# Kernel tuning notes

Hardware: AMD Instinct MI355X
Metric: run time of the kernel (lower is better)

## Reference

```python
import jax, jax.numpy as jnp
import numpy as np

N_NODES = 2048
N_ELEMS = 4096

# kind codes
KIND_R, KIND_IVS, KIND_VC, KIND_SW = 0, 1, 2, 3


def setup_inputs() -> dict:
    key = jax.random.key(0)
    k1, k2, k3 = jax.random.split(key, 3)
    M = jax.random.normal(k1, (N_NODES, N_ELEMS), dtype=jnp.float32)
    params = jax.random.uniform(k2, (N_ELEMS,), dtype=jnp.float32)
    kinds = jax.random.randint(k3, (N_ELEMS,), 0, 4, dtype=jnp.int32)
    return {"M": M, "params": params, "kinds": kinds}


def reference(M, params, kinds):
    N, E = M.shape
    W = 2 * E + N  # column width of every row block
    dt = M.dtype

    # kcl rows: [M | 0_{N,E} | 0_{N,N}]
    kcl = jnp.concatenate([M, jnp.zeros((N, E + N), dtype=dt)], axis=1)
    # kvl rows: [0_{E,E} | I_E | -M^T]
    kvl = jnp.concatenate(
        [jnp.zeros((E, E), dtype=dt), jnp.eye(E, dtype=dt), -M.T], axis=1
    )

    is_r = kinds == KIND_R
    is_ivs = kinds == KIND_IVS
    is_vc = kinds == KIND_VC
    is_sw = kinds == KIND_SW
    sw_on = params > 0

    one = jnp.ones((), dtype=dt)
    zero = jnp.zeros((), dtype=dt)
    # z-column value at pos: R -> -param, VC -> 1, SW(off) -> 1, else 0
    z_val = jnp.where(is_r, -params,
             jnp.where(is_vc | (is_sw & ~sw_on), one, zero)).astype(dt)
    # y-column value at E+pos: R -> 1, IVS -> 1, SW(on) -> 1, else 0
    y_val = jnp.where(is_r | is_ivs | (is_sw & sw_on), one, zero).astype(dt)

    pos = jnp.arange(E)
    elem = jnp.zeros((E, W), dtype=dt)
    elem = elem.at[pos, pos].set(z_val)
    elem = elem.at[pos, E + pos].set(y_val)

    return jnp.concatenate([kcl, kvl, elem], axis=0)
```

## Files before the change

kernel.cpp:

```cpp
#include <hip/hip_runtime.h>

#define NN 2048
#define EE 4096
#define WW 10240
#define TOT_ROWS 10240

typedef float v4f __attribute__((ext_vector_type(4)));

#define TP_BLOCKS 2048

__global__ __launch_bounds__(256) void coeff_kernel(
    const float* __restrict__ M,
    const float* __restrict__ params,
    const int*   __restrict__ kinds,
    float*       __restrict__ out)
{
    int tid = threadIdx.x;

    if (blockIdx.x < TP_BLOCKS) {
        __shared__ __align__(16) float t[64 * 64];
        int cTile = (blockIdx.x & 63) << 6;
        int rTile = (blockIdx.x >> 6) << 6;
        int r = tid & 15, q = tid >> 4;
        int c0 = r * 4;

        #pragma unroll
        for (int it = 0; it < 4; ++it) {
            int lrow = it * 16 + q;
            v4f val = *(const v4f*)(M + (size_t)(rTile + lrow) * EE + cTile + c0);
            *(v4f*)(out + (size_t)(rTile + lrow) * WW + cTile + c0) = val;
            #pragma unroll
            for (int s = 0; s < 4; ++s) {
                int i = (s + (r >> 2)) & 3;
                int c = c0 + i;
                t[c * 64 + (lrow ^ ((c & 15) * 4))] = val[i];
            }
        }
        __syncthreads();

        #pragma unroll
        for (int it = 0; it < 4; ++it) {
            int e  = it * 16 + q;
            int j0 = r * 4;
            v4f v = *(const v4f*)(t + e * 64 + (j0 ^ ((e & 15) * 4)));
            v4f nv = { -v[0], -v[1], -v[2], -v[3] };
            *(v4f*)(out + (size_t)(NN + cTile + e) * WW + 2 * EE + rTile + j0) = nv;
        }
    } else {
        int row = blockIdx.x - TP_BLOCKS;
        float* dst = out + (size_t)row * WW;
        const v4f zero = {0.f, 0.f, 0.f, 0.f};

        if (row < NN) {
            #pragma unroll
            for (int k = 4; k < 10; ++k)
                *(v4f*)(dst + (k * 256 + tid) * 4) = zero;
        } else if (row < NN + EE) {
            int e = row - NN;
            int col_y = EE + e;
            #pragma unroll
            for (int k = 0; k < 8; ++k) {
                int base = (k * 256 + tid) * 4;
                v4f v = zero;
                #pragma unroll
                for (int j = 0; j < 4; ++j)
                    if (base + j == col_y) v[j] = 1.0f;
                *(v4f*)(dst + base) = v;
            }
        } else {
            int e = row - (NN + EE);
            float p = params[e];
            int kk = kinds[e];
            bool on = p > 0.0f;
            float z, y;
            if (kk == 0)      { z = -p;             y = 1.0f; }
            else if (kk == 1) { z = 0.0f;           y = 1.0f; }
            else if (kk == 2) { z = 1.0f;           y = 0.0f; }
            else              { z = on ? 0.f : 1.f; y = on ? 1.f : 0.f; }
            int col_z = e, col_y = EE + e;
            #pragma unroll
            for (int k = 0; k < 10; ++k) {
                int base = (k * 256 + tid) * 4;
                v4f v = zero;
                #pragma unroll
                for (int j = 0; j < 4; ++j) {
                    if (base + j == col_z) v[j] = z;
                    if (base + j == col_y) v[j] = y;
                }
                *(v4f*)(dst + base) = v;
            }
        }
    }
}

extern "C" void kernel_launch(void* const* d_in, const int* in_sizes, int n_in,
                              void* d_out, int out_size, void* d_ws, size_t ws_size,
                              hipStream_t stream) {
    const float* M      = (const float*)d_in[0];
    const float* params = (const float*)d_in[1];
    const int*   kinds  = (const int*)d_in[2];
    float*       out    = (float*)d_out;

    coeff_kernel<<<TP_BLOCKS + TOT_ROWS, 256, 0, stream>>>(M, params, kinds, out);
}
```

Before: 434.2 us.

## Split into row-fill and transpose kernels with wider 64x256 transpose tiles

The single fused kernel becomes two launches. A row kernel writes every output row, including the copy of M into the KCL rows. A separate transpose kernel writes -M^T using 64x256 tiles held in 64KB of shared memory, so each output row segment is 1KB of contiguous stores instead of 256B. The cost is a second kernel launch with serialization between the two, lower occupancy from the larger shared memory tile, and M being read twice.

```diff
diff --git a/kernel.cpp b/kernel.cpp
--- a/kernel.cpp
+++ b/kernel.cpp
@@ -7,88 +7,101 @@
 
 typedef float v4f __attribute__((ext_vector_type(4)));
 
-#define TP_BLOCKS 2048
-
-__global__ __launch_bounds__(256) void coeff_kernel(
+__global__ __launch_bounds__(256) void row_kernel(
     const float* __restrict__ M,
     const float* __restrict__ params,
     const int*   __restrict__ kinds,
     float*       __restrict__ out)
 {
+    int row = blockIdx.x;
     int tid = threadIdx.x;
+    float* dst = out + (size_t)row * WW;
+    const v4f zero = {0.f, 0.f, 0.f, 0.f};
 
-    if (blockIdx.x < TP_BLOCKS) {
-        __shared__ __align__(16) float t[64 * 64];
-        int cTile = (blockIdx.x & 63) << 6;
-        int rTile = (blockIdx.x >> 6) << 6;
-        int r = tid & 15, q = tid >> 4;
-        int c0 = r * 4;
+    if (row < NN) {
+        const float* src = M + (size_t)row * EE;
+        #pragma unroll
+        for (int k = 0; k < 4; ++k) {
+            int off = (k * 256 + tid) * 4;
+            *(v4f*)(dst + off) = *(const v4f*)(src + off);
+        }
+        #pragma unroll
+        for (int k = 4; k < 10; ++k)
+            *(v4f*)(dst + (k * 256 + tid) * 4) = zero;
+    } else if (row < NN + EE) {
+        int e = row - NN;
+        int col_y = EE + e;
+        #pragma unroll
+        for (int k = 0; k < 8; ++k) {
+            int base = (k * 256 + tid) * 4;
+            v4f v = zero;
+            #pragma unroll
+            for (int j = 0; j < 4; ++j)
+                if (base + j == col_y) v[j] = 1.0f;
+            *(v4f*)(dst + base) = v;
+        }
+    } else {
+        int e = row - (NN + EE);
+        float p = params[e];
+        int kk = kinds[e];
+        bool on = p > 0.0f;
+        float z, y;
+        if (kk == 0)      { z = -p;             y = 1.0f; }
+        else if (kk == 1) { z = 0.0f;           y = 1.0f; }
+        else if (kk == 2) { z = 1.0f;           y = 0.0f; }
+        else              { z = on ? 0.f : 1.f; y = on ? 1.f : 0.f; }
+        int col_z = e, col_y = EE + e;
+        #pragma unroll
+        for (int k = 0; k < 10; ++k) {
+            int base = (k * 256 + tid) * 4;
+            v4f v = zero;
+            #pragma unroll
+            for (int j = 0; j < 4; ++j) {
+                if (base + j == col_z) v[j] = z;
+                if (base + j == col_y) v[j] = y;
+            }
+            *(v4f*)(dst + base) = v;
+        }
+    }
+}
 
+__global__ __launch_bounds__(256) void tp_kernel(
+    const float* __restrict__ M,
+    float*       __restrict__ out)
+{
+    __shared__ __align__(16) float t[4][64 * 64];
+    int cT = blockIdx.x << 6;
+    int rT = blockIdx.y << 8;
+    int tid = threadIdx.x;
+    int r = tid & 15, q = tid >> 4;
+    int c0 = r * 4;
+
+    #pragma unroll
+    for (int w = 0; w < 4; ++w) {
         #pragma unroll
         for (int it = 0; it < 4; ++it) {
             int lrow = it * 16 + q;
-            v4f val = *(const v4f*)(M + (size_t)(rTile + lrow) * EE + cTile + c0);
-            *(v4f*)(out + (size_t)(rTile + lrow) * WW + cTile + c0) = val;
+            v4f val = *(const v4f*)(M + (size_t)(rT + w * 64 + lrow) * EE + cT + c0);
             #pragma unroll
             for (int s = 0; s < 4; ++s) {
                 int i = (s + (r >> 2)) & 3;
                 int c = c0 + i;
-                t[c * 64 + (lrow ^ ((c & 15) * 4))] = val[i];
+                t[w][c * 64 + (lrow ^ ((c & 15) * 4))] = val[i];
             }
         }
-        __syncthreads();
+    }
+    __syncthreads();
 
+    #pragma unroll
+    for (int it = 0; it < 4; ++it) {
+        int e  = it * 16 + q;
+        int j0 = r * 4;
+        float* dst = out + (size_t)(NN + cT + e) * WW + 2 * EE + rT + j0;
         #pragma unroll
-        for (int it = 0; it < 4; ++it) {
-            int e  = it * 16 + q;
-            int j0 = r * 4;
-            v4f v = *(const v4f*)(t + e * 64 + (j0 ^ ((e & 15) * 4)));
+        for (int w = 0; w < 4; ++w) {
+            v4f v = *(const v4f*)(&t[w][e * 64 + (j0 ^ ((e & 15) * 4))]);
             v4f nv = { -v[0], -v[1], -v[2], -v[3] };
-            *(v4f*)(out + (size_t)(NN + cTile + e) * WW + 2 * EE + rTile + j0) = nv;
-        }
-    } else {
-        int row = blockIdx.x - TP_BLOCKS;
-        float* dst = out + (size_t)row * WW;
-        const v4f zero = {0.f, 0.f, 0.f, 0.f};
-
-        if (row < NN) {
-            #pragma unroll
-            for (int k = 4; k < 10; ++k)
-                *(v4f*)(dst + (k * 256 + tid) * 4) = zero;
-        } else if (row < NN + EE) {
-            int e = row - NN;
-            int col_y = EE + e;
-            #pragma unroll
-            for (int k = 0; k < 8; ++k) {
-                int base = (k * 256 + tid) * 4;
-                v4f v = zero;
-                #pragma unroll
-                for (int j = 0; j < 4; ++j)
-                    if (base + j == col_y) v[j] = 1.0f;
-                *(v4f*)(dst + base) = v;
-            }
-        } else {
-            int e = row - (NN + EE);
-            float p = params[e];
-            int kk = kinds[e];
-            bool on = p > 0.0f;
-            float z, y;
-            if (kk == 0)      { z = -p;             y = 1.0f; }
-            else if (kk == 1) { z = 0.0f;           y = 1.0f; }
-            else if (kk == 2) { z = 1.0f;           y = 0.0f; }
-            else              { z = on ? 0.f : 1.f; y = on ? 1.f : 0.f; }
-            int col_z = e, col_y = EE + e;
-            #pragma unroll
-            for (int k = 0; k < 10; ++k) {
-                int base = (k * 256 + tid) * 4;
-                v4f v = zero;
-                #pragma unroll
-                for (int j = 0; j < 4; ++j) {
-                    if (base + j == col_z) v[j] = z;
-                    if (base + j == col_y) v[j] = y;
-                }
-                *(v4f*)(dst + base) = v;
-            }
+            *(v4f*)(dst + w * 64) = nv;
         }
     }
 }
@@ -101,5 +114,6 @@
     const int*   kinds  = (const int*)d_in[2];
     float*       out    = (float*)d_out;
 
-    coeff_kernel<<<TP_BLOCKS + TOT_ROWS, 256, 0, stream>>>(M, params, kinds, out);
+    row_kernel<<<TOT_ROWS, 256, 0, stream>>>(M, params, kinds, out);
+    tp_kernel<<<dim3(EE / 64, NN / 256), 256, 0, stream>>>(M, out);
 }
```

Measured after the change: 443.5 us. 2.2% more time.

## Use nontemporal stores and enlarge transpose tiles to 64x256 per block

Applied to the files above, without the earlier changes.

All output writes now use nontemporal vector stores, to avoid polluting caches with the large write-only output. The transpose blocks each handle four 64x64 tiles along the node dimension, so each transposed row segment is 256 contiguous floats. This cuts the transpose block count by four. The larger shared buffer (64KB) reduces how many transpose blocks can be resident per CU.

```diff
diff --git a/kernel.cpp b/kernel.cpp
--- a/kernel.cpp
+++ b/kernel.cpp
@@ -7,7 +7,11 @@
 
 typedef float v4f __attribute__((ext_vector_type(4)));
 
-#define TP_BLOCKS 2048
+#define TP_BLOCKS 512
+
+__device__ __forceinline__ void nt_store(float* p, v4f v) {
+    __builtin_nontemporal_store(v, (v4f*)p);
+}
 
 __global__ __launch_bounds__(256) void coeff_kernel(
     const float* __restrict__ M,
@@ -18,22 +22,26 @@
     int tid = threadIdx.x;
 
     if (blockIdx.x < TP_BLOCKS) {
-        __shared__ __align__(16) float t[64 * 64];
-        int cTile = (blockIdx.x & 63) << 6;
-        int rTile = (blockIdx.x >> 6) << 6;
+        __shared__ __align__(16) float t[4][64 * 64];
+        int cT = (blockIdx.x & 63) << 6;
+        int rT = (blockIdx.x >> 6) << 8;
         int r = tid & 15, q = tid >> 4;
         int c0 = r * 4;
 
         #pragma unroll
-        for (int it = 0; it < 4; ++it) {
-            int lrow = it * 16 + q;
-            v4f val = *(const v4f*)(M + (size_t)(rTile + lrow) * EE + cTile + c0);
-            *(v4f*)(out + (size_t)(rTile + lrow) * WW + cTile + c0) = val;
+        for (int w = 0; w < 4; ++w) {
             #pragma unroll
-            for (int s = 0; s < 4; ++s) {
-                int i = (s + (r >> 2)) & 3;
-                int c = c0 + i;
-                t[c * 64 + (lrow ^ ((c & 15) * 4))] = val[i];
+            for (int it = 0; it < 4; ++it) {
+                int lrow = it * 16 + q;
+                int grow = rT + w * 64 + lrow;
+                v4f val = *(const v4f*)(M + (size_t)grow * EE + cT + c0);
+                nt_store(out + (size_t)grow * WW + cT + c0, val);
+                #pragma unroll
+                for (int s = 0; s < 4; ++s) {
+                    int i = (s + (r >> 2)) & 3;
+                    int c = c0 + i;
+                    t[w][c * 64 + (lrow ^ ((c & 15) * 4))] = val[i];
+                }
             }
         }
         __syncthreads();
@@ -42,30 +50,35 @@
         for (int it = 0; it < 4; ++it) {
             int e  = it * 16 + q;
             int j0 = r * 4;
-            v4f v = *(const v4f*)(t + e * 64 + (j0 ^ ((e & 15) * 4)));
-            v4f nv = { -v[0], -v[1], -v[2], -v[3] };
-            *(v4f*)(out + (size_t)(NN + cTile + e) * WW + 2 * EE + rTile + j0) = nv;
+            float* dst = out + (size_t)(NN + cT + e) * WW + 2 * EE + rT + j0;
+            #pragma unroll
+            for (int w = 0; w < 4; ++w) {
+                v4f v = *(const v4f*)(&t[w][e * 64 + (j0 ^ ((e & 15) * 4))]);
+                v4f nv = { -v[0], -v[1], -v[2], -v[3] };
+                nt_store(dst + w * 64, nv);
+            }
         }
     } else {
         int row = blockIdx.x - TP_BLOCKS;
+        int tid4 = tid * 4;
         float* dst = out + (size_t)row * WW;
         const v4f zero = {0.f, 0.f, 0.f, 0.f};
 
         if (row < NN) {
             #pragma unroll
             for (int k = 4; k < 10; ++k)
-                *(v4f*)(dst + (k * 256 + tid) * 4) = zero;
+                nt_store(dst + k * 1024 + tid4, zero);
         } else if (row < NN + EE) {
             int e = row - NN;
             int col_y = EE + e;
             #pragma unroll
             for (int k = 0; k < 8; ++k) {
-                int base = (k * 256 + tid) * 4;
+                int base = k * 1024 + tid4;
                 v4f v = zero;
                 #pragma unroll
                 for (int j = 0; j < 4; ++j)
                     if (base + j == col_y) v[j] = 1.0f;
-                *(v4f*)(dst + base) = v;
+                nt_store(dst + base, v);
             }
         } else {
             int e = row - (NN + EE);
@@ -80,14 +93,14 @@
             int col_z = e, col_y = EE + e;
             #pragma unroll
             for (int k = 0; k < 10; ++k) {
-                int base = (k * 256 + tid) * 4;
+                int base = k * 1024 + tid4;
                 v4f v = zero;
                 #pragma unroll
                 for (int j = 0; j < 4; ++j) {
                     if (base + j == col_z) v[j] = z;
                     if (base + j == col_y) v[j] = y;
                 }
-                *(v4f*)(dst + base) = v;
+                nt_store(dst + base, v);
             }
         }
     }
```

After: 429.2 us. Within noise of the previous version (-1.2%).
